# Performance work log

Measured on AMD Instinct MI355X. Metric: run time of the kernel, lower is better.

The kernel has to match this reference:

```python
import jax, jax.numpy as jnp
import numpy as np

N, E, G = 20000, 320000, 128
IN_C, H, H2, L = 128, 64, 128, 8
EPS_BN, EPS_MSG, EPS_SM = 1e-5, 1e-7, 1e-16


def _bn(x, g, b):
    # torch BatchNorm1d training-mode forward: biased batch statistics over nodes
    mu = jnp.mean(x, axis=0)
    var = jnp.mean((x - mu) ** 2, axis=0)
    return (x - mu) * jax.lax.rsqrt(var + EPS_BN) * g + b


def _seg_softmax(logits, idx, n):
    # numerically stable softmax over edges grouped by destination node
    m = jax.ops.segment_max(logits, idx, num_segments=n)
    e = jnp.exp(logits - m[idx])
    s = jax.ops.segment_sum(e, idx, num_segments=n)
    return e / (s[idx] + EPS_SM)


def _genconv(xs, xd, src, dst, ea, t, W1, b1, g1, bb1, W2, b2):
    # GENConv message: relu(x_j + edge_attr) + eps; softmax aggregation with temperature t
    msg = jax.nn.relu(xs[src] + ea) + EPS_MSG          # [E, H]
    alpha = _seg_softmax(msg * t, dst, N)              # [E, H]
    out = jax.ops.segment_sum(msg * alpha, dst, num_segments=N) + xd  # [N, H]
    # internal MLP (num_layers=2): Linear -> BN -> ReLU -> Linear
    h = jax.nn.relu(_bn(out @ W1 + b1, g1, bb1))       # [N, 2H]
    return h @ W2 + b2                                 # [N, H]


def _forward(x, edge_attr, src, dst, batch, W_src, b_src, W_dst, b_dst, W_edge, b_edge, t,
             mlp_W1, mlp_bias1, mlp_bn_g, mlp_bn_b, mlp_W2, mlp_bias2, norm_g, norm_b):
    # layer 0: conv only (in_channels != hidden -> lin_src / lin_dst projections)
    xs0 = x @ W_src + b_src
    xd0 = x @ W_dst + b_dst
    h = _genconv(xs0, xd0, src, dst, edge_attr @ W_edge[0] + b_edge[0], t[0],
                 mlp_W1[0], mlp_bias1[0], mlp_bn_g[0], mlp_bn_b[0], mlp_W2[0], mlp_bias2[0])
    # layers 1..7: res+ blocks  x + conv(act(norm(x)))   (dropout = identity in eval)
    for i in range(1, L):
        z = jax.nn.leaky_relu(_bn(h, norm_g[i], norm_b[i]))
        h = h + _genconv(z, z, src, dst, edge_attr @ W_edge[i] + b_edge[i], t[i],
                         mlp_W1[i], mlp_bias1[i], mlp_bn_g[i], mlp_bn_b[i], mlp_W2[i], mlp_bias2[i])
    # final norm/act of layer 0 applied to output, then global mean pool
    h = jax.nn.leaky_relu(_bn(h, norm_g[0], norm_b[0]))
    cnt = jnp.maximum(jax.ops.segment_sum(jnp.ones((N,), h.dtype), batch, num_segments=G), 1.0)
    return jax.ops.segment_sum(h, batch, num_segments=G) / cnt[:, None]


def setup_inputs() -> dict:
    key = jax.random.key(0)
    ks = jax.random.split(key, 10)
    x = jax.random.normal(ks[0], (N, IN_C), jnp.float32)
    edge_index = jax.random.randint(ks[1], (2, E), 0, N, dtype=jnp.int32)
    batch = jnp.sort(jax.random.randint(ks[2], (N,), 0, G, dtype=jnp.int32))
    edge_attr = jax.random.normal(ks[3], (E, 1), jnp.float32)

    def w(k, shape, fan):
        return jax.random.normal(k, shape, jnp.float32) / np.sqrt(fan).astype(np.float32)

    return {
        'x': x, 'edge_index': edge_index, 'batch': batch, 'edge_attr': edge_attr,
        'W_src': w(ks[4], (IN_C, H), IN_C), 'b_src': jnp.zeros((H,), jnp.float32),
        'W_dst': w(ks[5], (IN_C, H), IN_C), 'b_dst': jnp.zeros((H,), jnp.float32),
        'W_edge': w(ks[6], (L, 1, H), 1), 'b_edge': jnp.zeros((L, H), jnp.float32),
        't': jnp.full((L,), 0.1, jnp.float32),
        'mlp_W1': w(ks[7], (L, H, H2), H), 'mlp_bias1': jnp.zeros((L, H2), jnp.float32),
        'mlp_bn_g': jnp.ones((L, H2), jnp.float32), 'mlp_bn_b': jnp.zeros((L, H2), jnp.float32),
        'mlp_W2': w(ks[8], (L, H2, H), H2), 'mlp_bias2': jnp.zeros((L, H), jnp.float32),
        'norm_g': jnp.ones((L, H), jnp.float32), 'norm_b': jnp.zeros((L, H), jnp.float32),
    }


def reference(x, edge_index, batch, edge_attr, W_src, b_src, W_dst, b_dst, W_edge, b_edge, t,
              mlp_W1, mlp_bias1, mlp_bn_g, mlp_bn_b, mlp_W2, mlp_bias2, norm_g, norm_b):
    src, dst = edge_index[0], edge_index[1]
    return _forward(x, edge_attr, src, dst, batch, W_src, b_src, W_dst, b_dst, W_edge, b_edge, t,
                    mlp_W1, mlp_bias1, mlp_bn_g, mlp_bn_b, mlp_W2, mlp_bias2, norm_g, norm_b)
```

## Files before the change

kernel.cpp:

```cpp
#include <hip/hip_runtime.h>
#include <math.h>

#define N_NODES 20000
#define N_EDGES 320000
#define N_GRAPHS 128
#define L 8
#define NB 8
#define EPS_BN 1e-5f
#define EPS_MSG 1e-7f
#define EPS_SM 1e-16f
#define SLOPE 0.01f

__device__ __forceinline__ float leakyf(float x) { return x >= 0.f ? x : SLOPE * x; }

__device__ __forceinline__ void wave_sync_lds() {
  asm volatile("" ::: "memory");
  __builtin_amdgcn_wave_barrier();
  asm volatile("" ::: "memory");
}

__global__ void k_hist(const int* __restrict__ dst, int* __restrict__ counts) {
  int i = blockIdx.x * blockDim.x + threadIdx.x;
  if (i < N_EDGES) atomicAdd(&counts[dst[i]], 1);
}

__global__ __launch_bounds__(1024) void k_scan(const int* __restrict__ counts,
                                               int* __restrict__ row_ptr,
                                               int* __restrict__ cursor, int n) {
  __shared__ int psum[16];
  int tid = threadIdx.x;
  const int CHUNK = (n + 1023) / 1024;
  int start = tid * CHUNK;
  int end = start + CHUNK; if (end > n) end = n;
  int s = 0;
  for (int i = start; i < end; i++) s += counts[i];
  int lane = tid & 63, w = tid >> 6;
  int incl = s;
  for (int off = 1; off < 64; off <<= 1) {
    int u = __shfl_up(incl, off);
    if (lane >= off) incl += u;
  }
  if (lane == 63) psum[w] = incl;
  __syncthreads();
  int woff = 0;
  for (int k = 0; k < w; k++) woff += psum[k];
  int run = woff + incl - s;
  for (int i = start; i < end; i++) {
    row_ptr[i] = run; cursor[i] = run; run += counts[i];
  }
  if (tid == 1023) row_ptr[n] = run;
}

__global__ void k_scatter(const int* __restrict__ src, const int* __restrict__ dst,
                          const float* __restrict__ eattr, int* __restrict__ cursor,
                          int2* __restrict__ edata, int e) {
  int i = blockIdx.x * blockDim.x + threadIdx.x;
  if (i < e) {
    int d = dst[i];
    int pos = atomicAdd(&cursor[d], 1);
    edata[pos] = make_int2(src[i], __float_as_int(eattr[i]));
  }
}

__global__ __launch_bounds__(256) void k_lin0(const float* __restrict__ x,
                                              const float* __restrict__ Wsrc, const float* __restrict__ bsrc,
                                              const float* __restrict__ Wdst, const float* __restrict__ bdst,
                                              float* __restrict__ xs0, float* __restrict__ xd0) {
  __shared__ alignas(16) float xsh[4][NB][128];
  int tid = threadIdx.x, lane = tid & 63, w = tid >> 6;
  int l5 = lane & 31, jh = lane >> 5;
  int c2 = l5 * 2;
  float bs0 = bsrc[c2], bs1 = bsrc[c2 + 1], bd0 = bdst[c2], bd1 = bdst[c2 + 1];
  float as0[NB], as1[NB], ad0[NB], ad1[NB];
  int wave = blockIdx.x * 4 + w, nw = gridDim.x * 4;
  const int NBATCH = N_NODES / NB;
  for (int b = wave; b < NBATCH; b += nw) {
    int n0 = b * NB;
#pragma unroll
    for (int i = 0; i < NB; i++) {
      float2 xv = *(const float2*)&x[(n0 + i) * 128 + lane * 2];
      *(float2*)&xsh[w][i][lane * 2] = xv;
    }
    wave_sync_lds();
#pragma unroll
    for (int i = 0; i < NB; i++) { as0[i] = as1[i] = ad0[i] = ad1[i] = 0.f; }
    for (int j4 = 0; j4 < 16; j4++) {
      int j = jh * 64 + j4 * 4;
      float2 s0 = *(const float2*)&Wsrc[(j + 0) * 64 + c2];
      float2 s1 = *(const float2*)&Wsrc[(j + 1) * 64 + c2];
      float2 s2 = *(const float2*)&Wsrc[(j + 2) * 64 + c2];
      float2 s3 = *(const float2*)&Wsrc[(j + 3) * 64 + c2];
      float2 d0 = *(const float2*)&Wdst[(j + 0) * 64 + c2];
      float2 d1 = *(const float2*)&Wdst[(j + 1) * 64 + c2];
      float2 d2 = *(const float2*)&Wdst[(j + 2) * 64 + c2];
      float2 d3 = *(const float2*)&Wdst[(j + 3) * 64 + c2];
#pragma unroll
      for (int i = 0; i < NB; i++) {
        float4 o = *(const float4*)&xsh[w][i][j];
        as0[i] = fmaf(o.x, s0.x, as0[i]); as1[i] = fmaf(o.x, s0.y, as1[i]);
        ad0[i] = fmaf(o.x, d0.x, ad0[i]); ad1[i] = fmaf(o.x, d0.y, ad1[i]);
        as0[i] = fmaf(o.y, s1.x, as0[i]); as1[i] = fmaf(o.y, s1.y, as1[i]);
        ad0[i] = fmaf(o.y, d1.x, ad0[i]); ad1[i] = fmaf(o.y, d1.y, ad1[i]);
        as0[i] = fmaf(o.z, s2.x, as0[i]); as1[i] = fmaf(o.z, s2.y, as1[i]);
        ad0[i] = fmaf(o.z, d2.x, ad0[i]); ad1[i] = fmaf(o.z, d2.y, ad1[i]);
        as0[i] = fmaf(o.w, s3.x, as0[i]); as1[i] = fmaf(o.w, s3.y, as1[i]);
        ad0[i] = fmaf(o.w, d3.x, ad0[i]); ad1[i] = fmaf(o.w, d3.y, ad1[i]);
      }
    }
#pragma unroll
    for (int i = 0; i < NB; i++) {
      as0[i] += __shfl_xor(as0[i], 32); as1[i] += __shfl_xor(as1[i], 32);
      ad0[i] += __shfl_xor(ad0[i], 32); ad1[i] += __shfl_xor(ad1[i], 32);
    }
#pragma unroll
    for (int u = 0; u < 4; u++) {
      int i = jh * 4 + u;
      int n = n0 + i;
      *(float2*)&xs0[n * 64 + c2] = make_float2(as0[i] + bs0, as1[i] + bs1);
      *(float2*)&xd0[n * 64 + c2] = make_float2(ad0[i] + bd0, ad1[i] + bd1);
    }
  }
}

__global__ __launch_bounds__(256) void k_conv(
    const float* __restrict__ tbl_s, const float* __restrict__ tbl_d,
    const float* __restrict__ nstats, const float* __restrict__ ng,
    const float* __restrict__ nbv, int use_bn,
    const int* __restrict__ row_ptr, const int2* __restrict__ edata,
    const float* __restrict__ We, const float* __restrict__ be,
    const float* __restrict__ tptr,
    const float* __restrict__ W1, float* __restrict__ y1,
    float* __restrict__ stats ) {
  __shared__ alignas(16) float W1s[64 * 128];
  __shared__ alignas(16) float outs[4][NB][64];
  __shared__ float rsum[128], rsq[128];
  int tid = threadIdx.x, lane = tid & 63, w = tid >> 6;
  for (int i = tid; i < 64 * 128 / 4; i += 256)
    ((float4*)W1s)[i] = ((const float4*)W1)[i];
  if (tid < 128) { rsum[tid] = 0.f; rsq[tid] = 0.f; }
  __syncthreads();
  float sc = 1.f, sh = 0.f, slope = 1.f;
  if (use_bn) {
    const float inv = 1.f / N_NODES;
    float mu = nstats[lane] * inv;
    float var = nstats[64 + lane] * inv - mu * mu;
    sc = ng[lane] / sqrtf(var + EPS_BN);
    sh = nbv[lane] - mu * sc;
    slope = SLOPE;
  }
  float wec = We[lane], bec = be[lane], tval = tptr[0];
  int l5 = lane & 31, jh = lane >> 5;
  int c4 = l5 * 4;
  float acc[NB][4];
  float sA[4] = {0.f, 0.f, 0.f, 0.f}, qA[4] = {0.f, 0.f, 0.f, 0.f};
  int wave = blockIdx.x * 4 + w, nw = gridDim.x * 4;
  const int NBATCH = N_NODES / NB;
  for (int b = wave; b < NBATCH; b += nw) {
    int n0 = b * NB;
    for (int i = 0; i < NB; i++) {
      int n = n0 + i;
      int kb = row_ptr[n], ke = row_ptr[n + 1];
      float ssum = 0.f, wacc = 0.f;
#pragma unroll 8
      for (int k = kb; k < ke; k++) {
        int2 ed = edata[k];
        int sid = ed.x;
        float av = __int_as_float(ed.y);
        float hv = tbl_s[sid * 64 + lane];
        float zt = fmaf(hv, sc, sh);
        float zv = zt >= 0.f ? zt : zt * slope;
        float msg = fmaxf(zv + fmaf(av, wec, bec), 0.f) + EPS_MSG;
        float e = __expf(fminf(msg * tval, 60.f));
        ssum += e;
        wacc = fmaf(msg, e, wacc);
      }
      float dt = fmaf(tbl_d[n * 64 + lane], sc, sh);
      float dv = dt >= 0.f ? dt : dt * slope;
      outs[w][i][lane] = wacc / (ssum + EPS_SM) + dv;
    }
    wave_sync_lds();
#pragma unroll
    for (int i = 0; i < NB; i++)
#pragma unroll
      for (int c = 0; c < 4; c++) acc[i][c] = 0.f;
    for (int j4 = 0; j4 < 8; j4++) {
      int j = jh * 32 + j4 * 4;
      float4 w0 = *(const float4*)&W1s[(j + 0) * 128 + c4];
      float4 w1 = *(const float4*)&W1s[(j + 1) * 128 + c4];
      float4 w2 = *(const float4*)&W1s[(j + 2) * 128 + c4];
      float4 w3 = *(const float4*)&W1s[(j + 3) * 128 + c4];
#pragma unroll
      for (int i = 0; i < NB; i++) {
        float4 o = *(const float4*)&outs[w][i][j];
        acc[i][0] = fmaf(o.x, w0.x, acc[i][0]); acc[i][1] = fmaf(o.x, w0.y, acc[i][1]);
        acc[i][2] = fmaf(o.x, w0.z, acc[i][2]); acc[i][3] = fmaf(o.x, w0.w, acc[i][3]);
        acc[i][0] = fmaf(o.y, w1.x, acc[i][0]); acc[i][1] = fmaf(o.y, w1.y, acc[i][1]);
        acc[i][2] = fmaf(o.y, w1.z, acc[i][2]); acc[i][3] = fmaf(o.y, w1.w, acc[i][3]);
        acc[i][0] = fmaf(o.z, w2.x, acc[i][0]); acc[i][1] = fmaf(o.z, w2.y, acc[i][1]);
        acc[i][2] = fmaf(o.z, w2.z, acc[i][2]); acc[i][3] = fmaf(o.z, w2.w, acc[i][3]);
        acc[i][0] = fmaf(o.w, w3.x, acc[i][0]); acc[i][1] = fmaf(o.w, w3.y, acc[i][1]);
        acc[i][2] = fmaf(o.w, w3.z, acc[i][2]); acc[i][3] = fmaf(o.w, w3.w, acc[i][3]);
      }
    }
#pragma unroll
    for (int i = 0; i < NB; i++)
#pragma unroll
      for (int c = 0; c < 4; c++) acc[i][c] += __shfl_xor(acc[i][c], 32);
#pragma unroll
    for (int u = 0; u < 4; u++) {
      int i = jh * 4 + u;
      int n = n0 + i;
      float4 v = make_float4(acc[i][0], acc[i][1], acc[i][2], acc[i][3]);
      *(float4*)&y1[n * 128 + c4] = v;
      sA[0] += v.x; qA[0] += v.x * v.x;
      sA[1] += v.y; qA[1] += v.y * v.y;
      sA[2] += v.z; qA[2] += v.z * v.z;
      sA[3] += v.w; qA[3] += v.w * v.w;
    }
  }
#pragma unroll
  for (int c = 0; c < 4; c++) {
    atomicAdd(&rsum[c4 + c], sA[c]);
    atomicAdd(&rsq[c4 + c], qA[c]);
  }
  __syncthreads();
  if (tid < 128) {
    atomicAdd(&stats[tid], rsum[tid]);
    atomicAdd(&stats[128 + tid], rsq[tid]);
  }
}

__global__ __launch_bounds__(256) void k_mlp2(
    const float* __restrict__ y1, const float* __restrict__ ystats,
    const float* __restrict__ bng, const float* __restrict__ bnb,
    const float* __restrict__ W2, const float* __restrict__ b2,
    float* __restrict__ h, int add_res,
    float* __restrict__ hstats ) {
  __shared__ alignas(16) float W2s[128 * 64];
  __shared__ alignas(16) float h1s[4][NB][128];
  __shared__ float rsum[64], rsq[64];
  int tid = threadIdx.x, lane = tid & 63, w = tid >> 6;
  for (int i = tid; i < 128 * 64 / 4; i += 256)
    ((float4*)W2s)[i] = ((const float4*)W2)[i];
  if (tid < 64) { rsum[tid] = 0.f; rsq[tid] = 0.f; }
  __syncthreads();
  const float inv = 1.f / N_NODES;
  float mua = ystats[lane] * inv, mub = ystats[64 + lane] * inv;
  float va = ystats[128 + lane] * inv - mua * mua;
  float vb = ystats[192 + lane] * inv - mub * mub;
  float sca = bng[lane] / sqrtf(va + EPS_BN), scb = bng[64 + lane] / sqrtf(vb + EPS_BN);
  float sha = bnb[lane] - mua * sca, shb = bnb[64 + lane] - mub * scb;
  int l5 = lane & 31, jh = lane >> 5;
  int c2 = l5 * 2;
  float bias0 = b2[c2], bias1 = b2[c2 + 1];
  float acc0[NB], acc1[NB];
  float s0 = 0.f, q0 = 0.f, s1 = 0.f, q1 = 0.f;
  int wave = blockIdx.x * 4 + w, nw = gridDim.x * 4;
  const int NBATCH = N_NODES / NB;
  for (int b = wave; b < NBATCH; b += nw) {
    int n0 = b * NB;
#pragma unroll
    for (int i = 0; i < NB; i++) {
      int n = n0 + i;
      float va_ = y1[n * 128 + lane];
      float vb_ = y1[n * 128 + 64 + lane];
      h1s[w][i][lane] = fmaxf(fmaf(va_, sca, sha), 0.f);
      h1s[w][i][64 + lane] = fmaxf(fmaf(vb_, scb, shb), 0.f);
    }
    wave_sync_lds();
#pragma unroll
    for (int i = 0; i < NB; i++) { acc0[i] = 0.f; acc1[i] = 0.f; }
    for (int j4 = 0; j4 < 16; j4++) {
      int j = jh * 64 + j4 * 4;
      float2 w0 = *(const float2*)&W2s[(j + 0) * 64 + c2];
      float2 w1 = *(const float2*)&W2s[(j + 1) * 64 + c2];
      float2 w2v = *(const float2*)&W2s[(j + 2) * 64 + c2];
      float2 w3 = *(const float2*)&W2s[(j + 3) * 64 + c2];
#pragma unroll
      for (int i = 0; i < NB; i++) {
        float4 o = *(const float4*)&h1s[w][i][j];
        acc0[i] = fmaf(o.x, w0.x, acc0[i]); acc1[i] = fmaf(o.x, w0.y, acc1[i]);
        acc0[i] = fmaf(o.y, w1.x, acc0[i]); acc1[i] = fmaf(o.y, w1.y, acc1[i]);
        acc0[i] = fmaf(o.z, w2v.x, acc0[i]); acc1[i] = fmaf(o.z, w2v.y, acc1[i]);
        acc0[i] = fmaf(o.w, w3.x, acc0[i]); acc1[i] = fmaf(o.w, w3.y, acc1[i]);
      }
    }
#pragma unroll
    for (int i = 0; i < NB; i++) {
      acc0[i] += __shfl_xor(acc0[i], 32);
      acc1[i] += __shfl_xor(acc1[i], 32);
    }
#pragma unroll
    for (int u = 0; u < 4; u++) {
      int i = jh * 4 + u;
      int n = n0 + i;
      float v0 = acc0[i] + bias0, v1 = acc1[i] + bias1;
      if (add_res) {
        float2 ho = *(const float2*)&h[n * 64 + c2];
        v0 += ho.x; v1 += ho.y;
      }
      *(float2*)&h[n * 64 + c2] = make_float2(v0, v1);
      s0 += v0; q0 += v0 * v0;
      s1 += v1; q1 += v1 * v1;
    }
  }
  atomicAdd(&rsum[c2], s0); atomicAdd(&rsq[c2], q0);
  atomicAdd(&rsum[c2 + 1], s1); atomicAdd(&rsq[c2 + 1], q1);
  __syncthreads();
  if (tid < 64) {
    atomicAdd(&hstats[tid], rsum[tid]);
    atomicAdd(&hstats[64 + tid], rsq[tid]);
  }
}

__device__ __forceinline__ int lower_bound_i(const int* __restrict__ b, int n, int v) {
  int lo = 0, hi = n;
  while (lo < hi) { int mid = (lo + hi) >> 1; if (b[mid] < v) lo = mid + 1; else hi = mid; }
  return lo;
}

__global__ __launch_bounds__(256) void k_pool(const float* __restrict__ h,
                                              const float* __restrict__ hstats,
                                              const float* __restrict__ g0, const float* __restrict__ b0,
                                              const int* __restrict__ batch, float* __restrict__ out) {
  __shared__ float red[4][64];
  int g = blockIdx.x;
  int tid = threadIdx.x, lane = tid & 63, w = tid >> 6;
  int start = lower_bound_i(batch, N_NODES, g);
  int end = lower_bound_i(batch, N_NODES, g + 1);
  const float inv = 1.0f / N_NODES;
  float mu = hstats[lane] * inv;
  float var = hstats[64 + lane] * inv - mu * mu;
  float sc = g0[lane] / sqrtf(var + EPS_BN);
  float sh = b0[lane] - mu * sc;
  float acc = 0.f;
  for (int n = start + w; n < end; n += 4)
    acc += leakyf(fmaf(h[n * 64 + lane], sc, sh));
  red[w][lane] = acc;
  __syncthreads();
  if (w == 0) {
    float tot = red[0][lane] + red[1][lane] + red[2][lane] + red[3][lane];
    out[g * 64 + lane] = tot / fmaxf((float)(end - start), 1.0f);
  }
}

extern "C" void kernel_launch(void* const* d_in, const int* in_sizes, int n_in,
                              void* d_out, int out_size, void* d_ws, size_t ws_size,
                              hipStream_t stream) {
  const float* x      = (const float*)d_in[0];
  const int*   eidx   = (const int*)d_in[1];
  const int*   batch  = (const int*)d_in[2];
  const float* eattr  = (const float*)d_in[3];
  const float* Wsrc   = (const float*)d_in[4];
  const float* bsrc   = (const float*)d_in[5];
  const float* Wdst   = (const float*)d_in[6];
  const float* bdst   = (const float*)d_in[7];
  const float* Wedge  = (const float*)d_in[8];
  const float* bedge  = (const float*)d_in[9];
  const float* tparam = (const float*)d_in[10];
  const float* W1     = (const float*)d_in[11];
  const float* bng    = (const float*)d_in[13];
  const float* bnb    = (const float*)d_in[14];
  const float* W2     = (const float*)d_in[15];
  const float* b2     = (const float*)d_in[16];
  const float* ng     = (const float*)d_in[17];
  const float* nb     = (const float*)d_in[18];
  const int* srcp = eidx;
  const int* dstp = eidx + N_EDGES;

  char* ws = (char*)d_ws;
  size_t off = 0;
  auto alloc = [&](size_t bytes) {
    void* p = ws + off;
    off = (off + bytes + 255) & ~size_t(255);
    return p;
  };
  int*   counts   = (int*)alloc(N_NODES * 4);
  float* stats_y1 = (float*)alloc(L * 256 * 4);
  float* stats_h  = (float*)alloc(L * 128 * 4);
  size_t zero_bytes = off;
  int*   row_ptr    = (int*)alloc((N_NODES + 1) * 4);
  int*   cursor     = (int*)alloc(N_NODES * 4);
  int2*  edata      = (int2*)alloc(N_EDGES * 8);
  float* xs0        = (float*)alloc(N_NODES * 64 * 4);
  float* xd0        = (float*)alloc(N_NODES * 64 * 4);
  float* hbuf       = (float*)alloc(N_NODES * 64 * 4);
  float* y1         = (float*)alloc(N_NODES * 128 * 4);

  hipMemsetAsync(d_ws, 0, zero_bytes, stream);
  k_hist<<<(N_EDGES + 255) / 256, 256, 0, stream>>>(dstp, counts);
  k_scan<<<1, 1024, 0, stream>>>(counts, row_ptr, cursor, N_NODES);
  k_scatter<<<(N_EDGES + 255) / 256, 256, 0, stream>>>(srcp, dstp, eattr, cursor,
                                                       edata, N_EDGES);
  k_lin0<<<625, 256, 0, stream>>>(x, Wsrc, bsrc, Wdst, bdst, xs0, xd0);

  for (int i = 0; i < L; i++) {
    const float* xsp = (i == 0) ? xs0 : hbuf;
    const float* xdp = (i == 0) ? xd0 : hbuf;
    const float* nst = (i == 0) ? stats_h : stats_h + (i - 1) * 128;
    k_conv<<<625, 256, 0, stream>>>(xsp, xdp, nst, ng + i * 64, nb + i * 64, i > 0 ? 1 : 0,
                                    row_ptr, edata,
                                    Wedge + i * 64, bedge + i * 64, tparam + i,
                                    W1 + i * 64 * 128, y1, stats_y1 + i * 256);
    k_mlp2<<<625, 256, 0, stream>>>(y1, stats_y1 + i * 256, bng + i * 128, bnb + i * 128,
                                    W2 + i * 128 * 64, b2 + i * 64, hbuf, i > 0 ? 1 : 0,
                                    stats_h + i * 128);
  }
  k_pool<<<N_GRAPHS, 256, 0, stream>>>(hbuf, stats_h + 7 * 128, ng, nb, batch, (float*)d_out);
}
```

Before: 1.104 ms.

## Halve node batch per wave, load edge data cooperatively, read W2 from global

```diff
diff --git a/kernel.cpp b/kernel.cpp
--- a/kernel.cpp
+++ b/kernel.cpp
@@ -5,7 +5,8 @@
 #define N_EDGES 320000
 #define N_GRAPHS 128
 #define L 8
-#define NB 8
+#define NB0 8
+#define NBC 4
 #define EPS_BN 1e-5f
 #define EPS_MSG 1e-7f
 #define EPS_SM 1e-16f
@@ -66,24 +67,24 @@
                                               const float* __restrict__ Wsrc, const float* __restrict__ bsrc,
                                               const float* __restrict__ Wdst, const float* __restrict__ bdst,
                                               float* __restrict__ xs0, float* __restrict__ xd0) {
-  __shared__ alignas(16) float xsh[4][NB][128];
+  __shared__ alignas(16) float xsh[4][NB0][128];
   int tid = threadIdx.x, lane = tid & 63, w = tid >> 6;
   int l5 = lane & 31, jh = lane >> 5;
   int c2 = l5 * 2;
   float bs0 = bsrc[c2], bs1 = bsrc[c2 + 1], bd0 = bdst[c2], bd1 = bdst[c2 + 1];
-  float as0[NB], as1[NB], ad0[NB], ad1[NB];
+  float as0[NB0], as1[NB0], ad0[NB0], ad1[NB0];
   int wave = blockIdx.x * 4 + w, nw = gridDim.x * 4;
-  const int NBATCH = N_NODES / NB;
+  const int NBATCH = N_NODES / NB0;
   for (int b = wave; b < NBATCH; b += nw) {
-    int n0 = b * NB;
-#pragma unroll
-    for (int i = 0; i < NB; i++) {
+    int n0 = b * NB0;
+#pragma unroll
+    for (int i = 0; i < NB0; i++) {
       float2 xv = *(const float2*)&x[(n0 + i) * 128 + lane * 2];
       *(float2*)&xsh[w][i][lane * 2] = xv;
     }
     wave_sync_lds();
 #pragma unroll
-    for (int i = 0; i < NB; i++) { as0[i] = as1[i] = ad0[i] = ad1[i] = 0.f; }
+    for (int i = 0; i < NB0; i++) { as0[i] = as1[i] = ad0[i] = ad1[i] = 0.f; }
     for (int j4 = 0; j4 < 16; j4++) {
       int j = jh * 64 + j4 * 4;
       float2 s0 = *(const float2*)&Wsrc[(j + 0) * 64 + c2];
@@ -95,7 +96,7 @@
       float2 d2 = *(const float2*)&Wdst[(j + 2) * 64 + c2];
       float2 d3 = *(const float2*)&Wdst[(j + 3) * 64 + c2];
 #pragma unroll
-      for (int i = 0; i < NB; i++) {
+      for (int i = 0; i < NB0; i++) {
         float4 o = *(const float4*)&xsh[w][i][j];
         as0[i] = fmaf(o.x, s0.x, as0[i]); as1[i] = fmaf(o.x, s0.y, as1[i]);
         ad0[i] = fmaf(o.x, d0.x, ad0[i]); ad1[i] = fmaf(o.x, d0.y, ad1[i]);
@@ -108,7 +109,7 @@
       }
     }
 #pragma unroll
-    for (int i = 0; i < NB; i++) {
+    for (int i = 0; i < NB0; i++) {
       as0[i] += __shfl_xor(as0[i], 32); as1[i] += __shfl_xor(as1[i], 32);
       ad0[i] += __shfl_xor(ad0[i], 32); ad1[i] += __shfl_xor(ad1[i], 32);
     }
@@ -132,7 +133,7 @@
     const float* __restrict__ W1, float* __restrict__ y1,
     float* __restrict__ stats ) {
   __shared__ alignas(16) float W1s[64 * 128];
-  __shared__ alignas(16) float outs[4][NB][64];
+  __shared__ alignas(16) float outs[4][NBC][64];
   __shared__ float rsum[128], rsq[128];
   int tid = threadIdx.x, lane = tid & 63, w = tid >> 6;
   for (int i = tid; i < 64 * 128 / 4; i += 256)
@@ -151,36 +152,41 @@
   float wec = We[lane], bec = be[lane], tval = tptr[0];
   int l5 = lane & 31, jh = lane >> 5;
   int c4 = l5 * 4;
-  float acc[NB][4];
+  float acc[NBC][4];
   float sA[4] = {0.f, 0.f, 0.f, 0.f}, qA[4] = {0.f, 0.f, 0.f, 0.f};
   int wave = blockIdx.x * 4 + w, nw = gridDim.x * 4;
-  const int NBATCH = N_NODES / NB;
+  const int NBATCH = N_NODES / NBC;
   for (int b = wave; b < NBATCH; b += nw) {
-    int n0 = b * NB;
-    for (int i = 0; i < NB; i++) {
+    int n0 = b * NBC;
+    for (int i = 0; i < NBC; i++) {
       int n = n0 + i;
       int kb = row_ptr[n], ke = row_ptr[n + 1];
+      float dtv = tbl_d[n * 64 + lane];
       float ssum = 0.f, wacc = 0.f;
+      for (int k0 = kb; k0 < ke; k0 += 64) {
+        int idx = k0 + lane; if (idx >= ke) idx = ke - 1;
+        int2 my = edata[idx];
+        int cnt = ke - k0; if (cnt > 64) cnt = 64;
 #pragma unroll 8
-      for (int k = kb; k < ke; k++) {
-        int2 ed = edata[k];
-        int sid = ed.x;
-        float av = __int_as_float(ed.y);
-        float hv = tbl_s[sid * 64 + lane];
-        float zt = fmaf(hv, sc, sh);
-        float zv = zt >= 0.f ? zt : zt * slope;
-        float msg = fmaxf(zv + fmaf(av, wec, bec), 0.f) + EPS_MSG;
-        float e = __expf(fminf(msg * tval, 60.f));
-        ssum += e;
-        wacc = fmaf(msg, e, wacc);
+        for (int j = 0; j < cnt; j++) {
+          int sid = __shfl(my.x, j);
+          float av = __int_as_float(__shfl(my.y, j));
+          float hv = tbl_s[sid * 64 + lane];
+          float zt = fmaf(hv, sc, sh);
+          float zv = zt >= 0.f ? zt : zt * slope;
+          float msg = fmaxf(zv + fmaf(av, wec, bec), 0.f) + EPS_MSG;
+          float e = __expf(fminf(msg * tval, 60.f));
+          ssum += e;
+          wacc = fmaf(msg, e, wacc);
+        }
       }
-      float dt = fmaf(tbl_d[n * 64 + lane], sc, sh);
+      float dt = fmaf(dtv, sc, sh);
       float dv = dt >= 0.f ? dt : dt * slope;
       outs[w][i][lane] = wacc / (ssum + EPS_SM) + dv;
     }
     wave_sync_lds();
 #pragma unroll
-    for (int i = 0; i < NB; i++)
+    for (int i = 0; i < NBC; i++)
 #pragma unroll
       for (int c = 0; c < 4; c++) acc[i][c] = 0.f;
     for (int j4 = 0; j4 < 8; j4++) {
@@ -190,7 +196,7 @@
       float4 w2 = *(const float4*)&W1s[(j + 2) * 128 + c4];
       float4 w3 = *(const float4*)&W1s[(j + 3) * 128 + c4];
 #pragma unroll
-      for (int i = 0; i < NB; i++) {
+      for (int i = 0; i < NBC; i++) {
         float4 o = *(const float4*)&outs[w][i][j];
         acc[i][0] = fmaf(o.x, w0.x, acc[i][0]); acc[i][1] = fmaf(o.x, w0.y, acc[i][1]);
         acc[i][2] = fmaf(o.x, w0.z, acc[i][2]); acc[i][3] = fmaf(o.x, w0.w, acc[i][3]);
@@ -203,12 +209,12 @@
       }
     }
 #pragma unroll
-    for (int i = 0; i < NB; i++)
+    for (int i = 0; i < NBC; i++)
 #pragma unroll
       for (int c = 0; c < 4; c++) acc[i][c] += __shfl_xor(acc[i][c], 32);
 #pragma unroll
-    for (int u = 0; u < 4; u++) {
-      int i = jh * 4 + u;
+    for (int u = 0; u < 2; u++) {
+      int i = jh * 2 + u;
       int n = n0 + i;
       float4 v = make_float4(acc[i][0], acc[i][1], acc[i][2], acc[i][3]);
       *(float4*)&y1[n * 128 + c4] = v;
@@ -236,12 +242,9 @@
     const float* __restrict__ W2, const float* __restrict__ b2,
     float* __restrict__ h, int add_res,
     float* __restrict__ hstats ) {
-  __shared__ alignas(16) float W2s[128 * 64];
-  __shared__ alignas(16) float h1s[4][NB][128];
+  __shared__ alignas(16) float h1s[4][NBC][128];
   __shared__ float rsum[64], rsq[64];
   int tid = threadIdx.x, lane = tid & 63, w = tid >> 6;
-  for (int i = tid; i < 128 * 64 / 4; i += 256)
-    ((float4*)W2s)[i] = ((const float4*)W2)[i];
   if (tid < 64) { rsum[tid] = 0.f; rsq[tid] = 0.f; }
   __syncthreads();
   const float inv = 1.f / N_NODES;
@@ -253,14 +256,14 @@
   int l5 = lane & 31, jh = lane >> 5;
   int c2 = l5 * 2;
   float bias0 = b2[c2], bias1 = b2[c2 + 1];
-  float acc0[NB], acc1[NB];
+  float acc0[NBC], acc1[NBC];
   float s0 = 0.f, q0 = 0.f, s1 = 0.f, q1 = 0.f;
   int wave = blockIdx.x * 4 + w, nw = gridDim.x * 4;
-  const int NBATCH = N_NODES / NB;
+  const int NBATCH = N_NODES / NBC;
   for (int b = wave; b < NBATCH; b += nw) {
-    int n0 = b * NB;
-#pragma unroll
-    for (int i = 0; i < NB; i++) {
+    int n0 = b * NBC;
+#pragma unroll
+    for (int i = 0; i < NBC; i++) {
       int n = n0 + i;
       float va_ = y1[n * 128 + lane];
       float vb_ = y1[n * 128 + 64 + lane];
@@ -269,15 +272,15 @@
     }
     wave_sync_lds();
 #pragma unroll
-    for (int i = 0; i < NB; i++) { acc0[i] = 0.f; acc1[i] = 0.f; }
+    for (int i = 0; i < NBC; i++) { acc0[i] = 0.f; acc1[i] = 0.f; }
     for (int j4 = 0; j4 < 16; j4++) {
       int j = jh * 64 + j4 * 4;
-      float2 w0 = *(const float2*)&W2s[(j + 0) * 64 + c2];
-      float2 w1 = *(const float2*)&W2s[(j + 1) * 64 + c2];
-      float2 w2v = *(const float2*)&W2s[(j + 2) * 64 + c2];
-      float2 w3 = *(const float2*)&W2s[(j + 3) * 64 + c2];
-#pragma unroll
-      for (int i = 0; i < NB; i++) {
+      float2 w0 = *(const float2*)&W2[(j + 0) * 64 + c2];
+      float2 w1 = *(const float2*)&W2[(j + 1) * 64 + c2];
+      float2 w2v = *(const float2*)&W2[(j + 2) * 64 + c2];
+      float2 w3 = *(const float2*)&W2[(j + 3) * 64 + c2];
+#pragma unroll
+      for (int i = 0; i < NBC; i++) {
         float4 o = *(const float4*)&h1s[w][i][j];
         acc0[i] = fmaf(o.x, w0.x, acc0[i]); acc1[i] = fmaf(o.x, w0.y, acc1[i]);
         acc0[i] = fmaf(o.y, w1.x, acc0[i]); acc1[i] = fmaf(o.y, w1.y, acc1[i]);
@@ -286,13 +289,13 @@
       }
     }
 #pragma unroll
-    for (int i = 0; i < NB; i++) {
+    for (int i = 0; i < NBC; i++) {
       acc0[i] += __shfl_xor(acc0[i], 32);
       acc1[i] += __shfl_xor(acc1[i], 32);
     }
 #pragma unroll
-    for (int u = 0; u < 4; u++) {
-      int i = jh * 4 + u;
+    for (int u = 0; u < 2; u++) {
+      int i = jh * 2 + u;
       int n = n0 + i;
       float v0 = acc0[i] + bias0, v1 = acc1[i] + bias1;
       if (add_res) {
@@ -398,13 +401,13 @@
     const float* xsp = (i == 0) ? xs0 : hbuf;
     const float* xdp = (i == 0) ? xd0 : hbuf;
     const float* nst = (i == 0) ? stats_h : stats_h + (i - 1) * 128;
-    k_conv<<<625, 256, 0, stream>>>(xsp, xdp, nst, ng + i * 64, nb + i * 64, i > 0 ? 1 : 0,
-                                    row_ptr, edata,
-                                    Wedge + i * 64, bedge + i * 64, tparam + i,
-                                    W1 + i * 64 * 128, y1, stats_y1 + i * 256);
-    k_mlp2<<<625, 256, 0, stream>>>(y1, stats_y1 + i * 256, bng + i * 128, bnb + i * 128,
-                                    W2 + i * 128 * 64, b2 + i * 64, hbuf, i > 0 ? 1 : 0,
-                                    stats_h + i * 128);
+    k_conv<<<1250, 256, 0, stream>>>(xsp, xdp, nst, ng + i * 64, nb + i * 64, i > 0 ? 1 : 0,
+                                     row_ptr, edata,
+                                     Wedge + i * 64, bedge + i * 64, tparam + i,
+                                     W1 + i * 64 * 128, y1, stats_y1 + i * 256);
+    k_mlp2<<<1250, 256, 0, stream>>>(y1, stats_y1 + i * 256, bng + i * 128, bnb + i * 128,
+                                     W2 + i * 128 * 64, b2 + i * 64, hbuf, i > 0 ? 1 : 0,
+                                     stats_h + i * 128);
   }
   k_pool<<<N_GRAPHS, 256, 0, stream>>>(hbuf, stats_h + 7 * 128, ng, nb, batch, (float*)d_out);
 }
```

New measurement: 1.238 ms. 12.1% more time.
